# Performance work log

Hardware: AMD Instinct MI355X
Metric: run time of the kernel (lower is better)

## Reference

```python
import jax, jax.numpy as jnp
import numpy as np

C = 19
D = 128
TAU_HARD = 0.2
EMA = 0.999
BETA = 0.7
TH_I, TH_F = 0.5, 0.85
TL_I, TL_F = 0.1, 0.3
EPS = 1e-7


def _l2norm(x, axis):
    n = jnp.linalg.norm(x, axis=axis, keepdims=True)
    return x / jnp.maximum(n, 1e-12)


def _flatten_feat(feat):
    # [B,D,Hf,Wf] -> [N,D]
    B, Dd, Hf, Wf = feat.shape
    return feat.transpose(0, 2, 3, 1).reshape(-1, Dd)


def _build_protos(feat, labels, weights=None):
    # single-pass segment reduce replacing the per-class python loop
    f = _flatten_feat(feat)
    seg = labels.reshape(-1)
    w = jnp.ones(seg.shape, f.dtype) if weights is None else weights.reshape(-1)
    wsum_f = jax.ops.segment_sum(w[:, None] * f, seg, num_segments=C)  # [C,D]
    wsum = jax.ops.segment_sum(w, seg, num_segments=C)                 # [C]
    cnt = jax.ops.segment_sum(jnp.ones_like(w), seg, num_segments=C)
    proto = wsum_f / (wsum[:, None] + EPS)
    return proto, cnt >= 1.0


def _hard_contrastive(feat, labels, mem, mem_init):
    f = _l2norm(_flatten_feat(feat), axis=1)          # [N,D]
    lab = labels.reshape(-1)
    valid = mem_init[lab].astype(f.dtype)
    logits = (f @ mem.T) / TAU_HARD                   # [N,C]
    ce = -jnp.take_along_axis(jax.nn.log_softmax(logits, axis=1), lab[:, None], axis=1)[:, 0]
    nv = jnp.sum(valid)
    return jnp.where(nv > 0, jnp.sum(ce * valid) / jnp.maximum(nv, 1.0), 0.0)


def _ce_map(logits, target):
    # per-pixel cross entropy, logits [B,C,H,W], target [B,H,W]
    ls = jax.nn.log_softmax(logits, axis=1)
    return -jnp.take_along_axis(ls, target[:, None], axis=1)[:, 0]


def setup_inputs() -> dict:
    key = jax.random.key(0)
    ks = jax.random.split(key, 9)
    B, Hf, Wf = 4, 128, 128
    H = W = 512
    f = lambda k: jax.random.normal(k, (B, D, Hf, Wf), jnp.float32)
    g = lambda k: jax.random.normal(k, (B, C, H, W), jnp.float32)
    return {
        "feat_l1": f(ks[0]), "feat_l2": f(ks[1]),
        "feat_u1": f(ks[2]), "feat_u2": f(ks[3]),
        "logits_l1": g(ks[4]), "logits_l2": g(ks[5]),
        "logits_u1": g(ks[6]), "logits_u2": g(ks[7]),
        "memory": jnp.zeros((C, D), jnp.float32),
        "gt_labels": jax.random.randint(ks[8], (B, H, W), 0, C),
        "memory_init": jnp.zeros((C,), bool),
        "cur_iter": 10000,
        "max_iter": 40000,
    }


def reference(feat_l1, feat_l2, feat_u1, feat_u2, logits_l1, logits_l2,
              logits_u1, logits_u2, memory, gt_labels, memory_init,
              cur_iter, max_iter):
    B, _, Hf, Wf = feat_l1.shape
    H, W = logits_u1.shape[2], logits_u1.shape[3]

    q_u1 = jax.nn.softmax(logits_u1, axis=1)
    q_u2 = jax.nn.softmax(logits_u2, axis=1)

    # reliability r_u [B,H,W]
    y1 = jnp.argmax(q_u1, axis=1)
    y2 = jnp.argmax(q_u2, axis=1)
    agree = (y1 == y2).astype(q_u1.dtype)
    conf = (jnp.max(q_u1, axis=1) + jnp.max(q_u2, axis=1)) / 2.0
    m = (q_u1 + q_u2) / 2.0
    logm = jnp.log(jnp.maximum(m, EPS))
    kl1 = jnp.sum(q_u1 * (jnp.log(jnp.maximum(q_u1, EPS)) - logm), axis=1)
    kl2 = jnp.sum(q_u2 * (jnp.log(jnp.maximum(q_u2, EPS)) - logm), axis=1)
    r_u = agree * conf * jnp.exp(-(kl1 + kl2) / 2.0)

    # cosine-annealed thresholds
    ratio = float(cur_iter) / max(int(max_iter), 1)
    tau_high = TH_F - (TH_F - TH_I) * np.cos(np.pi * ratio / 2)

    # UCPS (pseudo labels are argmax of logits == argmax of softmax)
    loss_ucps = jnp.mean(jax.lax.stop_gradient(r_u) * (_ce_map(logits_u1, y2) + _ce_map(logits_u2, y1)))

    # nearest downsample (integer stride, matches torch nearest floor indexing)
    ih = jnp.arange(Hf) * (H // Hf)
    iw = jnp.arange(Wf) * (W // Wf)
    gt_down = gt_labels[:, ih][:, :, iw]
    pseudo_consensus = jnp.where(y1 != y2, 0, y1)
    pseudo_u_down = pseudo_consensus[:, ih][:, :, iw]
    # bilinear (align_corners=False == half-pixel, no antialias)
    r_u_down = jax.image.resize(r_u, (B, Hf, Wf), method='linear', antialias=False)

    anchor_mask = r_u_down > tau_high

    feat_l = (feat_l1 + feat_l2) / 2.0
    feat_u = (feat_u1 + feat_u2) / 2.0
    pl, pl_pres = _build_protos(feat_l, gt_down)
    anchor_r = jnp.where(anchor_mask, r_u_down, 0.0)
    pu, pu_pres = _build_protos(feat_u, pseudo_u_down, anchor_r)

    both = pl_pres & pu_pres
    merged = jnp.where(both[:, None], BETA * pl + (1.0 - BETA) * pu,
                       jnp.where(pl_pres[:, None], pl, pu))
    present = pl_pres | pu_pres
    merged = jax.lax.stop_gradient(merged)  # update_memory is no_grad

    p_norm = _l2norm(merged, axis=1)
    ema = _l2norm(EMA * memory + (1.0 - EMA) * p_norm, axis=1)
    new_mem = jnp.where((present & ~memory_init)[:, None], p_norm,
                        jnp.where((present & memory_init)[:, None], ema, memory))
    new_init = memory_init | present
    new_mem = jax.lax.stop_gradient(new_mem)

    loss_hard_l = (_hard_contrastive(feat_l1, gt_down, new_mem, new_init)
                   + _hard_contrastive(feat_l2, gt_down, new_mem, new_init)) / 2.0
    # contrastive_mode == 'all_hard'
    loss_hard_u = (_hard_contrastive(feat_u1, pseudo_u_down, new_mem, new_init)
                   + _hard_contrastive(feat_u2, pseudo_u_down, new_mem, new_init)) / 2.0

    loss_dgpc = loss_hard_l + loss_hard_u  # loss_soft == 0 in all_hard mode
    return jnp.stack([loss_dgpc, loss_ucps])
```

## Files before the change

kernel.cpp:

```cpp
#include <hip/hip_runtime.h>
#include <math.h>

#define NCLS 19
#define DD   128
#define EPSV 1e-7f
#define LOGEPS -16.118095651f

#define OFF_TAU    0
#define OFF_CNTL   8
#define OFF_WSUMU  32
#define OFF_CNTU   64
#define OFF_CE     96
#define OFF_VALID  100
#define OFF_UCPS   104
#define OFF_SUML   128
#define OFF_SUMU   2560
#define OFF_MEM    4992
#define OFF_INIT   7424
#define OFF_RUD    7456
#define OFF_PSEUDO 72992
#define ZERO_N     72992

__device__ __forceinline__ void fatom(float* p, float v) { unsafeAtomicAdd(p, v); }

__global__ __launch_bounds__(256) void kZ(float* __restrict__ W,
                                          const int* __restrict__ cur_it,
                                          const int* __restrict__ max_it) {
    int i = blockIdx.x * 256 + threadIdx.x;
    if (i == 0) {
        int mi = max_it[0]; if (mi < 1) mi = 1;
        double ratio = (double)cur_it[0] / (double)mi;
        W[OFF_TAU] = (float)(0.85 - (0.85 - 0.5) * cos(M_PI * ratio * 0.5));
    } else if (i < ZERO_N) {
        W[i] = 0.0f;
    }
}

__global__ __launch_bounds__(256) void kB(const float* __restrict__ lu1,
                                          const float* __restrict__ lu2,
                                          float* __restrict__ W) {
    float* rud = W + OFF_RUD;
    int* pseudo = (int*)(W + OFF_PSEUDO);
    int t = blockIdx.x * 256 + threadIdx.x;
    int b = t >> 18;
    int rem = t & 262143;
    int h = rem >> 9, w = rem & 511;
    const float* p1 = lu1 + (size_t)b * (NCLS * 262144) + rem;
    const float* p2 = lu2 + (size_t)b * (NCLS * 262144) + rem;

    float v1[NCLS], v2[NCLS];
#pragma unroll
    for (int c = 0; c < NCLS; c++) v1[c] = p1[(size_t)c * 262144];
#pragma unroll
    for (int c = 0; c < NCLS; c++) v2[c] = p2[(size_t)c * 262144];

    float m1 = v1[0]; int y1 = 0;
    float m2 = v2[0]; int y2 = 0;
#pragma unroll
    for (int c = 1; c < NCLS; c++) {
        if (v1[c] > m1) { m1 = v1[c]; y1 = c; }
        if (v2[c] > m2) { m2 = v2[c]; y2 = c; }
    }
    float s1 = 0.f, s2 = 0.f;
#pragma unroll
    for (int c = 0; c < NCLS; c++) { s1 += __expf(v1[c] - m1); s2 += __expf(v2[c] - m2); }
    float lse1 = m1 + __logf(s1);
    float lse2 = m2 + __logf(s2);

    float kl = 0.f, l1y2 = v1[0], l2y1 = v2[0];
#pragma unroll
    for (int c = 0; c < NCLS; c++) {
        float lq1 = v1[c] - lse1, lq2 = v2[c] - lse2;
        float q1 = __expf(lq1), q2 = __expf(lq2);
        float mm = 0.5f * (q1 + q2);
        float lm = __logf(fmaxf(mm, EPSV));
        kl += q1 * (fmaxf(lq1, LOGEPS) - lm) + q2 * (fmaxf(lq2, LOGEPS) - lm);
        if (c == y2) l1y2 = v1[c];
        if (c == y1) l2y1 = v2[c];
    }
    float conf = 0.5f * (1.f / s1 + 1.f / s2);
    float r_u = (y1 == y2) ? conf * __expf(-0.5f * kl) : 0.f;
    float ce = (lse1 - l1y2) + (lse2 - l2y1);
    float contrib = r_u * ce;

    __shared__ float red[256];
    red[threadIdx.x] = contrib;
    __syncthreads();
    for (int s = 128; s > 0; s >>= 1) {
        if (threadIdx.x < s) red[threadIdx.x] += red[threadIdx.x + s];
        __syncthreads();
    }
    if (threadIdx.x == 0) fatom(&W[OFF_UCPS], red[0]);

    int hm = h & 3, wm = w & 3;
    if ((hm == 1 || hm == 2) && (wm == 1 || wm == 2))
        fatom(&rud[b * 16384 + (h >> 2) * 128 + (w >> 2)], 0.25f * r_u);
    if (hm == 0 && wm == 0)
        pseudo[b * 16384 + (h >> 2) * 128 + (w >> 2)] = (y1 == y2) ? y1 : 0;
}

__global__ __launch_bounds__(256) void kC(const float* __restrict__ fl1,
                                          const float* __restrict__ fl2,
                                          const float* __restrict__ fu1,
                                          const float* __restrict__ fu2,
                                          const int* __restrict__ gt,
                                          float* __restrict__ W) {
    __shared__ float tile[DD * 33];
    __shared__ float accL[2 * NCLS * DD];
    __shared__ float accU[2 * NCLS * DD];
    __shared__ int   sLab[32], sCu[32];
    __shared__ float sW[32];
    __shared__ float sCntL[NCLS], sCntU[NCLS], sWUs[NCLS];
    __shared__ int   sAny;

    int tid = threadIdx.x;
    for (int i = tid; i < 2 * NCLS * DD; i += 256) { accL[i] = 0.f; accU[i] = 0.f; }
    if (tid < NCLS) { sCntL[tid] = 0.f; sCntU[tid] = 0.f; sWUs[tid] = 0.f; }
    if (tid == 0) sAny = 0;
    __syncthreads();

    int P0 = blockIdx.x * 128;
    int b = P0 >> 14;
    const float tau = W[OFF_TAU];
    const float* rud = W + OFF_RUD;
    const int* pseudo = (const int*)(W + OFF_PSEUDO);
    size_t gb = (size_t)b * 2097152;

    int d = tid & 127, pg = tid >> 7;

    for (int T = 0; T < 4; T++) {
        int rem0 = (P0 + T * 32) & 16383;
        if (tid < 32) {
            int rem = rem0 + tid;
            int bp = b * 16384 + rem;
            int ii = rem >> 7, jj = rem & 127;
            int cl = gt[b * 262144 + ii * 2048 + jj * 4];
            int cu = pseudo[bp];
            float rd = rud[bp];
            float w = (rd > tau) ? rd : 0.f;
            sLab[tid] = cl; sCu[tid] = cu; sW[tid] = w;
            fatom(&sCntL[cl], 1.f);
            fatom(&sCntU[cu], 1.f);
            if (w > 0.f) { fatom(&sWUs[cu], w); sAny = 1; }
        }
        for (int i = tid; i < 32 * DD; i += 256) {
            int dd = i >> 5, p = i & 31;
            size_t g = gb + (size_t)dd * 16384 + rem0 + p;
            tile[dd * 33 + p] = 0.5f * (fl1[g] + fl2[g]);
        }
        __syncthreads();
        float* aL = &accL[pg * (NCLS * DD) + d];
        float* aU = &accU[pg * (NCLS * DD) + d];
#pragma unroll
        for (int p = pg * 16; p < pg * 16 + 16; p++) {
            int c = sLab[p];
            aL[c * DD] += tile[d * 33 + p];
            float w = sW[p];
            if (w > 0.f) {
                size_t g = gb + (size_t)d * 16384 + rem0 + p;
                aU[sCu[p] * DD] += w * 0.5f * (fu1[g] + fu2[g]);
            }
        }
        __syncthreads();
    }
    for (int i = tid; i < NCLS * DD; i += 256)
        fatom(&W[OFF_SUML + i], accL[i] + accL[NCLS * DD + i]);
    if (sAny)
        for (int i = tid; i < NCLS * DD; i += 256)
            fatom(&W[OFF_SUMU + i], accU[i] + accU[NCLS * DD + i]);
    if (tid < NCLS) {
        fatom(&W[OFF_CNTL + tid], sCntL[tid]);
        fatom(&W[OFF_WSUMU + tid], sWUs[tid]);
        fatom(&W[OFF_CNTU + tid], sCntU[tid]);
    }
}

__global__ __launch_bounds__(128) void kD(const float* __restrict__ mem,
                                          const unsigned char* __restrict__ minit,
                                          float* __restrict__ W) {
    int c = blockIdx.x, d = threadIdx.x;
    __shared__ float red[128];
    float cntL = W[OFF_CNTL + c], wsU = W[OFF_WSUMU + c], cntU = W[OFF_CNTU + c];
    bool plp = cntL >= 1.f, pup = cntU >= 1.f;
    float pl = W[OFF_SUML + c * DD + d] / (cntL + EPSV);
    float pu = W[OFF_SUMU + c * DD + d] / (wsU + EPSV);
    float merged = (plp && pup) ? (0.7f * pl + 0.3f * pu) : (plp ? pl : pu);

    red[d] = merged * merged; __syncthreads();
    for (int s = 64; s > 0; s >>= 1) { if (d < s) red[d] += red[d + s]; __syncthreads(); }
    float nrm = red[0];
    __syncthreads();
    float pn = merged / fmaxf(sqrtf(nrm), 1e-12f);

    float mo = mem[c * DD + d];
    float e = 0.999f * mo + 0.001f * pn;
    red[d] = e * e; __syncthreads();
    for (int s = 64; s > 0; s >>= 1) { if (d < s) red[d] += red[d + s]; __syncthreads(); }
    float ne = red[0];
    float ema = e / fmaxf(sqrtf(ne), 1e-12f);

    bool present = plp || pup;
    bool init = (minit[c] != 0);
    float nm = present ? (init ? ema : pn) : mo;
    W[OFF_MEM + c * DD + d] = nm;
    if (d == 0) W[OFF_INIT + c] = (init || present) ? 1.f : 0.f;
}

__device__ __forceinline__ void pix_loss(const float dots[NCLS], float nn, int lab,
                                         const float* sInit, float& ce_acc, float& v_acc) {
    float inv = 5.0f / fmaxf(sqrtf(nn), 1e-12f);
    float lg[NCLS];
#pragma unroll
    for (int c = 0; c < NCLS; c++) lg[c] = dots[c] * inv;
    float mx = lg[0];
#pragma unroll
    for (int c = 1; c < NCLS; c++) mx = fmaxf(mx, lg[c]);
    float s = 0.f;
#pragma unroll
    for (int c = 0; c < NCLS; c++) s += __expf(lg[c] - mx);
    float lse = mx + __logf(s);
    float ll = lg[0];
#pragma unroll
    for (int c = 1; c < NCLS; c++) if (c == lab) ll = lg[c];
    float vld = sInit[lab];
    ce_acc += vld * (lse - ll);
    v_acc += vld;
}

__global__ __launch_bounds__(256) void kE(const float* __restrict__ f0,
                                          const float* __restrict__ f1,
                                          const float* __restrict__ f2,
                                          const float* __restrict__ f3,
                                          const int* __restrict__ gt,
                                          float* __restrict__ W) {
    __shared__ __align__(16) float sMem[NCLS * DD];
    __shared__ float sInit[NCLS];
    __shared__ float redA[256], redB[256];
    int fid = blockIdx.y;
    const float* feat = (fid == 0) ? f0 : (fid == 1) ? f1 : (fid == 2) ? f2 : f3;
    for (int i = threadIdx.x; i < NCLS * DD; i += 256) sMem[i] = W[OFF_MEM + i];
    if (threadIdx.x < NCLS) sInit[threadIdx.x] = W[OFF_INIT + threadIdx.x];
    __syncthreads();

    int p0 = blockIdx.x * 512 + threadIdx.x;
    int b = p0 >> 14;
    int rem0 = p0 & 16383;
    const float* fp = feat + (size_t)b * 2097152 + rem0;

    float dots0[NCLS], dots1[NCLS];
#pragma unroll
    for (int c = 0; c < NCLS; c++) { dots0[c] = 0.f; dots1[c] = 0.f; }
    float n0 = 0.f, n1 = 0.f;

    for (int d0 = 0; d0 < DD; d0 += 4) {
        const float* fpp = fp + (size_t)d0 * 16384;
        float a0 = fpp[0],     a1 = fpp[16384],       a2 = fpp[32768],       a3 = fpp[49152];
        float b0 = fpp[256],   b1 = fpp[16384 + 256], b2 = fpp[32768 + 256], b3 = fpp[49152 + 256];
        n0 += a0 * a0 + a1 * a1 + a2 * a2 + a3 * a3;
        n1 += b0 * b0 + b1 * b1 + b2 * b2 + b3 * b3;
#pragma unroll
        for (int c = 0; c < NCLS; c++) {
            float4 mv = *(const float4*)&sMem[c * DD + d0];
            dots0[c] += a0 * mv.x + a1 * mv.y + a2 * mv.z + a3 * mv.w;
            dots1[c] += b0 * mv.x + b1 * mv.y + b2 * mv.z + b3 * mv.w;
        }
    }

    const int* pseudo = (const int*)(W + OFF_PSEUDO);
    int rem1 = rem0 + 256;
    int lab0 = (fid < 2) ? gt[b * 262144 + (rem0 >> 7) * 2048 + (rem0 & 127) * 4] : pseudo[p0];
    int lab1 = (fid < 2) ? gt[b * 262144 + (rem1 >> 7) * 2048 + (rem1 & 127) * 4] : pseudo[p0 + 256];

    float ce_acc = 0.f, v_acc = 0.f;
    pix_loss(dots0, n0, lab0, sInit, ce_acc, v_acc);
    pix_loss(dots1, n1, lab1, sInit, ce_acc, v_acc);

    redA[threadIdx.x] = ce_acc;
    redB[threadIdx.x] = v_acc;
    __syncthreads();
    for (int s = 128; s > 0; s >>= 1) {
        if (threadIdx.x < s) { redA[threadIdx.x] += redA[threadIdx.x + s]; redB[threadIdx.x] += redB[threadIdx.x + s]; }
        __syncthreads();
    }
    if (threadIdx.x == 0) {
        fatom(&W[OFF_CE + fid], redA[0]);
        fatom(&W[OFF_VALID + fid], redB[0]);
    }
}

__global__ void kF(float* __restrict__ out, const float* __restrict__ W) {
    if (threadIdx.x == 0 && blockIdx.x == 0) {
        float h[4];
#pragma unroll
        for (int i = 0; i < 4; i++) {
            float nv = W[OFF_VALID + i];
            h[i] = (nv > 0.f) ? W[OFF_CE + i] / fmaxf(nv, 1.f) : 0.f;
        }
        out[0] = 0.5f * (h[0] + h[1]) + 0.5f * (h[2] + h[3]);
        out[1] = W[OFF_UCPS] * (1.0f / 1048576.0f);
    }
}

extern "C" void kernel_launch(void* const* d_in, const int* in_sizes, int n_in,
                              void* d_out, int out_size, void* d_ws, size_t ws_size,
                              hipStream_t stream) {
    const float* fl1 = (const float*)d_in[0];
    const float* fl2 = (const float*)d_in[1];
    const float* fu1 = (const float*)d_in[2];
    const float* fu2 = (const float*)d_in[3];
    const float* lu1 = (const float*)d_in[6];
    const float* lu2 = (const float*)d_in[7];
    const float* mem = (const float*)d_in[8];
    const int* gt = (const int*)d_in[9];
    const unsigned char* minit = (const unsigned char*)d_in[10];
    const int* cur = (const int*)d_in[11];
    const int* mxi = (const int*)d_in[12];
    float* W = (float*)d_ws;
    float* out = (float*)d_out;

    kZ<<<286, 256, 0, stream>>>(W, cur, mxi);
    kB<<<4096, 256, 0, stream>>>(lu1, lu2, W);
    kC<<<512, 256, 0, stream>>>(fl1, fl2, fu1, fu2, gt, W);
    kD<<<NCLS, 128, 0, stream>>>(mem, minit, W);
    kE<<<dim3(128, 4), 256, 0, stream>>>(fl1, fl2, fu1, fu2, gt, W);
    kF<<<1, 64, 0, stream>>>(out, W);
}
```

Before: 430.1 us.

## Vectorize logits kernel to four pixels per thread and widen feature loads

The pseudo-label kernel now has each thread handle four adjacent pixels through float4 loads, with a wave-shuffle reduction and fewer atomics, and it launches a quarter as many blocks. The prototype kernel loads its feature tile with float4 and drops the shared unlabeled accumulator in favour of direct global atomics. The contrastive kernel loads eight channels per step instead of four. The aim is better memory-load efficiency and lower LDS use, at the cost of much higher register pressure in kB and possible global atomic contention in kC.

```diff
diff --git a/kernel.cpp b/kernel.cpp
--- a/kernel.cpp
+++ b/kernel.cpp
@@ -36,67 +36,82 @@
     }
 }
 
-__global__ __launch_bounds__(256) void kB(const float* __restrict__ lu1,
-                                          const float* __restrict__ lu2,
-                                          float* __restrict__ W) {
+__global__ __launch_bounds__(256, 2) void kB(const float* __restrict__ lu1,
+                                             const float* __restrict__ lu2,
+                                             float* __restrict__ W) {
     float* rud = W + OFF_RUD;
     int* pseudo = (int*)(W + OFF_PSEUDO);
     int t = blockIdx.x * 256 + threadIdx.x;
-    int b = t >> 18;
-    int rem = t & 262143;
-    int h = rem >> 9, w = rem & 511;
-    const float* p1 = lu1 + (size_t)b * (NCLS * 262144) + rem;
-    const float* p2 = lu2 + (size_t)b * (NCLS * 262144) + rem;
-
-    float v1[NCLS], v2[NCLS];
-#pragma unroll
-    for (int c = 0; c < NCLS; c++) v1[c] = p1[(size_t)c * 262144];
-#pragma unroll
-    for (int c = 0; c < NCLS; c++) v2[c] = p2[(size_t)c * 262144];
-
-    float m1 = v1[0]; int y1 = 0;
-    float m2 = v2[0]; int y2 = 0;
-#pragma unroll
-    for (int c = 1; c < NCLS; c++) {
-        if (v1[c] > m1) { m1 = v1[c]; y1 = c; }
-        if (v2[c] > m2) { m2 = v2[c]; y2 = c; }
-    }
-    float s1 = 0.f, s2 = 0.f;
-#pragma unroll
-    for (int c = 0; c < NCLS; c++) { s1 += __expf(v1[c] - m1); s2 += __expf(v2[c] - m2); }
-    float lse1 = m1 + __logf(s1);
-    float lse2 = m2 + __logf(s2);
-
-    float kl = 0.f, l1y2 = v1[0], l2y1 = v2[0];
-#pragma unroll
-    for (int c = 0; c < NCLS; c++) {
-        float lq1 = v1[c] - lse1, lq2 = v2[c] - lse2;
-        float q1 = __expf(lq1), q2 = __expf(lq2);
-        float mm = 0.5f * (q1 + q2);
-        float lm = __logf(fmaxf(mm, EPSV));
-        kl += q1 * (fmaxf(lq1, LOGEPS) - lm) + q2 * (fmaxf(lq2, LOGEPS) - lm);
-        if (c == y2) l1y2 = v1[c];
-        if (c == y1) l2y1 = v2[c];
-    }
-    float conf = 0.5f * (1.f / s1 + 1.f / s2);
-    float r_u = (y1 == y2) ? conf * __expf(-0.5f * kl) : 0.f;
-    float ce = (lse1 - l1y2) + (lse2 - l2y1);
-    float contrib = r_u * ce;
-
-    __shared__ float red[256];
-    red[threadIdx.x] = contrib;
-    __syncthreads();
-    for (int s = 128; s > 0; s >>= 1) {
-        if (threadIdx.x < s) red[threadIdx.x] += red[threadIdx.x + s];
-        __syncthreads();
-    }
-    if (threadIdx.x == 0) fatom(&W[OFF_UCPS], red[0]);
-
-    int hm = h & 3, wm = w & 3;
-    if ((hm == 1 || hm == 2) && (wm == 1 || wm == 2))
-        fatom(&rud[b * 16384 + (h >> 2) * 128 + (w >> 2)], 0.25f * r_u);
-    if (hm == 0 && wm == 0)
-        pseudo[b * 16384 + (h >> 2) * 128 + (w >> 2)] = (y1 == y2) ? y1 : 0;
+    int b = t >> 16;
+    int rem4 = (t << 2) & 262143;
+    int h = rem4 >> 9, w0 = rem4 & 511;
+
+    const float4* p1 = (const float4*)lu1 + (size_t)b * (NCLS * 65536) + (rem4 >> 2);
+    const float4* p2 = (const float4*)lu2 + (size_t)b * (NCLS * 65536) + (rem4 >> 2);
+
+    float4 v1[NCLS], v2[NCLS];
+#pragma unroll
+    for (int c = 0; c < NCLS; c++) v1[c] = p1[c * 65536];
+#pragma unroll
+    for (int c = 0; c < NCLS; c++) v2[c] = p2[c * 65536];
+    const float* a1 = (const float*)v1;
+    const float* a2 = (const float*)v2;
+
+    float contrib = 0.f;
+    float ru12 = 0.f;
+    int pl0 = 0;
+
+#pragma unroll
+    for (int e = 0; e < 4; e++) {
+        float m1 = a1[e]; int y1 = 0;
+        float m2 = a2[e]; int y2 = 0;
+#pragma unroll
+        for (int c = 1; c < NCLS; c++) {
+            float x1 = a1[c * 4 + e], x2 = a2[c * 4 + e];
+            if (x1 > m1) { m1 = x1; y1 = c; }
+            if (x2 > m2) { m2 = x2; y2 = c; }
+        }
+        float s1 = 0.f, s2 = 0.f;
+#pragma unroll
+        for (int c = 0; c < NCLS; c++) {
+            s1 += __expf(a1[c * 4 + e] - m1);
+            s2 += __expf(a2[c * 4 + e] - m2);
+        }
+        float lse1 = m1 + __logf(s1);
+        float lse2 = m2 + __logf(s2);
+
+        float kl = 0.f, l1y2 = a1[e], l2y1 = a2[e];
+#pragma unroll
+        for (int c = 0; c < NCLS; c++) {
+            float x1 = a1[c * 4 + e], x2 = a2[c * 4 + e];
+            float lq1 = x1 - lse1, lq2 = x2 - lse2;
+            float q1 = __expf(lq1), q2 = __expf(lq2);
+            float mm = 0.5f * (q1 + q2);
+            float lm = __logf(fmaxf(mm, EPSV));
+            kl += q1 * (fmaxf(lq1, LOGEPS) - lm) + q2 * (fmaxf(lq2, LOGEPS) - lm);
+            if (c == y2) l1y2 = x1;
+            if (c == y1) l2y1 = x2;
+        }
+        float conf = 0.5f * (1.f / s1 + 1.f / s2);
+        float r_u = (y1 == y2) ? conf * __expf(-0.5f * kl) : 0.f;
+        float ce = (lse1 - l1y2) + (lse2 - l2y1);
+        contrib += r_u * ce;
+        if (e == 1 || e == 2) ru12 += r_u;
+        if (e == 0) pl0 = (y1 == y2) ? y1 : 0;
+    }
+
+    float cs = contrib;
+#pragma unroll
+    for (int o = 32; o > 0; o >>= 1) cs += __shfl_down(cs, o, 64);
+    __shared__ float wsum[4];
+    if ((threadIdx.x & 63) == 0) wsum[threadIdx.x >> 6] = cs;
+    __syncthreads();
+    if (threadIdx.x == 0) fatom(&W[OFF_UCPS], wsum[0] + wsum[1] + wsum[2] + wsum[3]);
+
+    int hm = h & 3;
+    int didx = b * 16384 + (h >> 2) * 128 + (w0 >> 2);
+    if (hm == 1 || hm == 2) fatom(&rud[didx], 0.25f * ru12);
+    if (hm == 0) pseudo[didx] = pl0;
 }
 
 __global__ __launch_bounds__(256) void kC(const float* __restrict__ fl1,
@@ -107,16 +122,13 @@
                                           float* __restrict__ W) {
     __shared__ float tile[DD * 33];
     __shared__ float accL[2 * NCLS * DD];
-    __shared__ float accU[2 * NCLS * DD];
     __shared__ int   sLab[32], sCu[32];
     __shared__ float sW[32];
     __shared__ float sCntL[NCLS], sCntU[NCLS], sWUs[NCLS];
-    __shared__ int   sAny;
 
     int tid = threadIdx.x;
-    for (int i = tid; i < 2 * NCLS * DD; i += 256) { accL[i] = 0.f; accU[i] = 0.f; }
+    for (int i = tid; i < 2 * NCLS * DD; i += 256) accL[i] = 0.f;
     if (tid < NCLS) { sCntL[tid] = 0.f; sCntU[tid] = 0.f; sWUs[tid] = 0.f; }
-    if (tid == 0) sAny = 0;
     __syncthreads();
 
     int P0 = blockIdx.x * 128;
@@ -141,16 +153,21 @@
             sLab[tid] = cl; sCu[tid] = cu; sW[tid] = w;
             fatom(&sCntL[cl], 1.f);
             fatom(&sCntU[cu], 1.f);
-            if (w > 0.f) { fatom(&sWUs[cu], w); sAny = 1; }
-        }
-        for (int i = tid; i < 32 * DD; i += 256) {
-            int dd = i >> 5, p = i & 31;
-            size_t g = gb + (size_t)dd * 16384 + rem0 + p;
-            tile[dd * 33 + p] = 0.5f * (fl1[g] + fl2[g]);
+            if (w > 0.f) fatom(&sWUs[cu], w);
+        }
+        for (int i = tid; i < 1024; i += 256) {
+            int dd = i >> 3, p4 = (i & 7) << 2;
+            size_t g = gb + (size_t)dd * 16384 + rem0 + p4;
+            float4 x1 = *(const float4*)(fl1 + g);
+            float4 x2 = *(const float4*)(fl2 + g);
+            float* tp = &tile[dd * 33 + p4];
+            tp[0] = 0.5f * (x1.x + x2.x);
+            tp[1] = 0.5f * (x1.y + x2.y);
+            tp[2] = 0.5f * (x1.z + x2.z);
+            tp[3] = 0.5f * (x1.w + x2.w);
         }
         __syncthreads();
         float* aL = &accL[pg * (NCLS * DD) + d];
-        float* aU = &accU[pg * (NCLS * DD) + d];
 #pragma unroll
         for (int p = pg * 16; p < pg * 16 + 16; p++) {
             int c = sLab[p];
@@ -158,16 +175,13 @@
             float w = sW[p];
             if (w > 0.f) {
                 size_t g = gb + (size_t)d * 16384 + rem0 + p;
-                aU[sCu[p] * DD] += w * 0.5f * (fu1[g] + fu2[g]);
+                fatom(&W[OFF_SUMU + sCu[p] * DD + d], w * 0.5f * (fu1[g] + fu2[g]));
             }
         }
         __syncthreads();
     }
     for (int i = tid; i < NCLS * DD; i += 256)
         fatom(&W[OFF_SUML + i], accL[i] + accL[NCLS * DD + i]);
-    if (sAny)
-        for (int i = tid; i < NCLS * DD; i += 256)
-            fatom(&W[OFF_SUMU + i], accU[i] + accU[NCLS * DD + i]);
     if (tid < NCLS) {
         fatom(&W[OFF_CNTL + tid], sCntL[tid]);
         fatom(&W[OFF_WSUMU + tid], sWUs[tid]);
@@ -252,17 +266,24 @@
     for (int c = 0; c < NCLS; c++) { dots0[c] = 0.f; dots1[c] = 0.f; }
     float n0 = 0.f, n1 = 0.f;
 
-    for (int d0 = 0; d0 < DD; d0 += 4) {
+    for (int d0 = 0; d0 < DD; d0 += 8) {
         const float* fpp = fp + (size_t)d0 * 16384;
-        float a0 = fpp[0],     a1 = fpp[16384],       a2 = fpp[32768],       a3 = fpp[49152];
-        float b0 = fpp[256],   b1 = fpp[16384 + 256], b2 = fpp[32768 + 256], b3 = fpp[49152 + 256];
-        n0 += a0 * a0 + a1 * a1 + a2 * a2 + a3 * a3;
-        n1 += b0 * b0 + b1 * b1 + b2 * b2 + b3 * b3;
+        float a[8], bb[8];
+#pragma unroll
+        for (int j = 0; j < 8; j++) {
+            a[j]  = fpp[(size_t)j * 16384];
+            bb[j] = fpp[(size_t)j * 16384 + 256];
+        }
+#pragma unroll
+        for (int j = 0; j < 8; j++) { n0 += a[j] * a[j]; n1 += bb[j] * bb[j]; }
 #pragma unroll
         for (int c = 0; c < NCLS; c++) {
-            float4 mv = *(const float4*)&sMem[c * DD + d0];
-            dots0[c] += a0 * mv.x + a1 * mv.y + a2 * mv.z + a3 * mv.w;
-            dots1[c] += b0 * mv.x + b1 * mv.y + b2 * mv.z + b3 * mv.w;
+            float4 m0 = *(const float4*)&sMem[c * DD + d0];
+            float4 m1 = *(const float4*)&sMem[c * DD + d0 + 4];
+            dots0[c] += a[0] * m0.x + a[1] * m0.y + a[2] * m0.z + a[3] * m0.w
+                      + a[4] * m1.x + a[5] * m1.y + a[6] * m1.z + a[7] * m1.w;
+            dots1[c] += bb[0] * m0.x + bb[1] * m0.y + bb[2] * m0.z + bb[3] * m0.w
+                      + bb[4] * m1.x + bb[5] * m1.y + bb[6] * m1.z + bb[7] * m1.w;
         }
     }
 
@@ -319,7 +340,7 @@
     float* out = (float*)d_out;
 
     kZ<<<286, 256, 0, stream>>>(W, cur, mxi);
-    kB<<<4096, 256, 0, stream>>>(lu1, lu2, W);
+    kB<<<1024, 256, 0, stream>>>(lu1, lu2, W);
     kC<<<512, 256, 0, stream>>>(fl1, fl2, fu1, fu2, gt, W);
     kD<<<NCLS, 128, 0, stream>>>(mem, minit, W);
     kE<<<dim3(128, 4), 256, 0, stream>>>(fl1, fl2, fu1, fu2, gt, W);
```

Result: faster. 418.1 us (-2.8%).
